# Performance work log

Hardware: AMD Instinct MI355X
Metric: run time of the kernel (lower is better)

The kernel has to match this reference:

```python
import jax, jax.numpy as jnp
import numpy as np

S_LOCAL = 3
N_HEADS = 8
EPS = 1e-6


def setup_inputs() -> dict:
    key = jax.random.key(0)
    ks = jax.random.split(key, 9)
    B, D, T, H, W = 2, 512, 96, 16, 16
    std = 0.02
    return {
        "x": jax.random.normal(ks[0], (B, D, T, H, W), dtype=jnp.float32),
        "ln_gamma": jnp.ones((D,), dtype=jnp.float32),
        "ln_beta": jnp.zeros((D,), dtype=jnp.float32),
        "Wq": jax.random.normal(ks[1], (D, D), dtype=jnp.float32) * std,
        "Wk": jax.random.normal(ks[2], (D, D), dtype=jnp.float32) * std,
        "Wv": jax.random.normal(ks[3], (D, D), dtype=jnp.float32) * std,
        "Wkl": jax.random.normal(ks[4], (D, D), dtype=jnp.float32) * std,
        "Wvl": jax.random.normal(ks[5], (D, D), dtype=jnp.float32) * std,
        "Wo": jax.random.normal(ks[6], (D, D), dtype=jnp.float32) * std,
        "q_bias": jax.random.normal(ks[7], (1, N_HEADS, 1, D // N_HEADS), dtype=jnp.float32) * std,
    }


def _unfold_windows(x, s):
    # x: [..., T] -> [..., T, s] sliding windows with zero padding s//2 each side
    p = s // 2
    xp = jnp.pad(x, [(0, 0)] * (x.ndim - 1) + [(p, p)])
    T = x.shape[-1]
    idx = jnp.arange(T)[:, None] + jnp.arange(s)[None, :]  # [T, s]
    return xp[..., idx]


def reference(x, ln_gamma, ln_beta, Wq, Wk, Wv, Wkl, Wvl, Wo, q_bias):
    B, D, T, H, W = x.shape
    nh, dh, s = N_HEADS, D // N_HEADS, S_LOCAL
    factor = dh ** (-0.5)
    N = B * H * W

    # [B,D,T,H,W] -> [N, T, D]
    xt = jnp.transpose(x, (0, 3, 4, 2, 1)).reshape(N, T, D)

    # LayerNorm over D
    mu = xt.mean(-1, keepdims=True)
    var = xt.var(-1, keepdims=True)
    xn = (xt - mu) / jnp.sqrt(var + EPS) * ln_gamma + ln_beta

    # projections -> [N, nh, T, dh]
    def heads(y):
        return jnp.transpose(y.reshape(N, T, nh, dh), (0, 2, 1, 3))

    q = heads(xn @ Wq.T) + q_bias
    k = heads(xn @ Wk.T)
    v = heads(xn @ Wv.T)

    # global attention scores [N, nh, T, T]
    attn_global = jnp.einsum('bhnd,bhgd->bhng', q, k) * factor

    # local k/v: [N, T, D] -> [N, D, T] -> windows [N, D, T, s]
    kl = jnp.transpose(xn @ Wkl.T, (0, 2, 1))
    vl = jnp.transpose(xn @ Wvl.T, (0, 2, 1))
    k_w = jnp.transpose(_unfold_windows(kl, s).reshape(N, nh, dh, T, s), (0, 1, 3, 2, 4))  # [N,nh,T,dh,s]
    v_w = jnp.transpose(_unfold_windows(vl, s).reshape(N, nh, dh, T, s), (0, 1, 3, 2, 4))

    # local mask: True where window element came from zero padding -> [T, s]
    mask_local = _unfold_windows(jnp.ones((T,), dtype=jnp.float32), s) == 0

    attn_local = jnp.einsum('bhnd,bhndl->bhnl', q, k_w)
    attn_local = jnp.where(mask_local, -jnp.inf, attn_local) * factor

    # joint softmax over [T global + s local]
    attn_map = jax.nn.softmax(jnp.concatenate([attn_global, attn_local], axis=-1), axis=-1)
    ag, al = attn_map[..., :T], attn_map[..., T:]

    x_global = jnp.einsum('bhng,bhgd->bhnd', ag, v)
    x_local = jnp.einsum('bhnl,bhndl->bhnd', al, v_w)

    out = (jnp.transpose(x_global + x_local, (0, 2, 1, 3)).reshape(N, T, D)) @ Wo.T
    return jnp.transpose(out.reshape(B, H, W, T, D), (0, 4, 3, 1, 2))
```

## Files before the change

kernel.cpp:

```cpp
#include <hip/hip_runtime.h>
#include <hip/hip_fp16.h>
#include <cstdint>
#include <cstddef>

typedef _Float16 f16;
typedef _Float16 half8 __attribute__((ext_vector_type(8)));
typedef _Float16 half4v __attribute__((ext_vector_type(4)));
typedef float floatx4 __attribute__((ext_vector_type(4)));

#define MTOT 49152

__device__ __forceinline__ void gload_lds16(const f16* g, f16* l) {
  __builtin_amdgcn_global_load_lds((const __attribute__((address_space(1))) void*)g,
                                   (__attribute__((address_space(3))) void*)l, 16, 0, 0);
}

__device__ __forceinline__ half8 load_h8u(const f16* p) {
  half8 v;
  __builtin_memcpy(&v, p, 16);
  return v;
}

__global__ __launch_bounds__(256) void wconv_kernel(
    const float* __restrict__ Wq, const float* __restrict__ Wk,
    const float* __restrict__ Wv, const float* __restrict__ Wkl,
    const float* __restrict__ Wvl, const float* __restrict__ Wo,
    f16* __restrict__ WQKV, f16* __restrict__ WO) {
  int idx = blockIdx.x * 256 + threadIdx.x;
  if (idx < 2560 * 512) {
    int row = idx >> 9;
    int col = idx & 511;
    int seg = row >> 9;
    int r = row & 511;
    const float* src;
    switch (seg) {
      case 0: src = Wq; break;
      case 1: src = Wk; break;
      case 2: src = Wkl; break;
      case 3: src = Wvl; break;
      default: src = Wv; break;
    }
    WQKV[idx] = (f16)src[r * 512 + col];
  }
  if (idx < 512 * 512) WO[idx] = (f16)Wo[idx];
}

__global__ __launch_bounds__(256) void ln_kernel(
    const float* __restrict__ x, const float* __restrict__ gamma,
    const float* __restrict__ beta, f16* __restrict__ XN) {
  const int hwg = blockIdx.x & 3;
  const int t   = (blockIdx.x >> 2) % 96;
  const int b   = blockIdx.x / (4 * 96);
  const int lhw = threadIdx.x & 63;
  const int dg  = threadIdx.x >> 6;
  const int hw  = hwg * 64 + lhw;
  const float* xp = x + (size_t)b * 512 * 24576 + (size_t)t * 256 + hw;

  float s = 0.f, s2 = 0.f;
  for (int d = dg * 128; d < dg * 128 + 128; ++d) {
    float v = xp[(size_t)d * 24576];
    s += v;
    s2 += v * v;
  }
  __shared__ float S1[4][64], S2[4][64];
  S1[dg][lhw] = s;
  S2[dg][lhw] = s2;
  __syncthreads();
  s  = S1[0][lhw] + S1[1][lhw] + S1[2][lhw] + S1[3][lhw];
  s2 = S2[0][lhw] + S2[1][lhw] + S2[2][lhw] + S2[3][lhw];
  const float mean = s * (1.f / 512.f);
  float var = s2 * (1.f / 512.f) - mean * mean;
  var = fmaxf(var, 0.f);
  const float rstd = rsqrtf(var + 1e-6f);
  const int n = b * 256 + hw;
  f16* outp = XN + ((size_t)n * 96 + t) * 512;
  for (int d0 = dg * 128; d0 < dg * 128 + 128; d0 += 8) {
    half8 buf;
#pragma unroll
    for (int j = 0; j < 8; ++j) {
      float v = xp[(size_t)(d0 + j) * 24576];
      buf[j] = (f16)((v - mean) * rstd * gamma[d0 + j] + beta[d0 + j]);
    }
    *(half8*)(outp + d0) = buf;
  }
}

template <int EPI>
__global__ __launch_bounds__(256) void gemm_kernel(
    const f16* __restrict__ A, const f16* __restrict__ B,
    f16* __restrict__ Cqkv, f16* __restrict__ VT, f16* __restrict__ VLT,
    const float* __restrict__ qbias, float* __restrict__ Out) {
  __shared__ f16 As[2][128 * 32];
  __shared__ f16 Bs[2][128 * 32];
  __shared__ f16 esc[4][16][20];

  const int lin = blockIdx.x;
  const int cpx = (int)gridDim.x >> 3;
  const int o = (lin & 7) * cpx + (lin >> 3);
  int mt, nt;
  if (EPI == 0) {
    mt = o / 20;
    nt = o % 20;
  } else {
    nt = o >> 2;
    mt = o & 3;
  }
  const int m0 = mt * 128;
  const int n0 = nt * 128;
  const int tid = threadIdx.x;
  const int lane = tid & 63;
  const int wid = tid >> 6;
  const int wm = wid >> 1, wn = wid & 1;
  const int l15 = lane & 15, l4 = lane >> 4;

  floatx4 acc[4][4] = {};

  const int srow = tid >> 2;
  const int skp = (((tid & 3) ^ ((tid >> 3) & 3))) * 8;
  const f16* ap = A + (size_t)(m0 + srow) * 512 + skp;
  const f16* bp = B + (size_t)(n0 + srow) * 512 + skp;

  auto stage = [&](int buf, int k0) {
    f16* asl = As[buf] + tid * 8;
    f16* bsl = Bs[buf] + tid * 8;
    gload_lds16(ap + k0, asl);
    gload_lds16(ap + (size_t)64 * 512 + k0, asl + 2048);
    gload_lds16(bp + k0, bsl);
    gload_lds16(bp + (size_t)64 * 512 + k0, bsl + 2048);
  };

  const int rc = (l4 ^ ((l15 >> 1) & 3)) * 8;

  stage(0, 0);
  __syncthreads();
  int cur = 0;
  for (int k0 = 0; k0 < 512; k0 += 32) {
    if (k0 + 32 < 512) stage(cur ^ 1, k0 + 32);
    half8 af[4], bf[4];
#pragma unroll
    for (int mf = 0; mf < 4; ++mf)
      af[mf] = *(const half8*)(As[cur] + (wm * 64 + mf * 16 + l15) * 32 + rc);
#pragma unroll
    for (int nf = 0; nf < 4; ++nf)
      bf[nf] = *(const half8*)(Bs[cur] + (wn * 64 + nf * 16 + l15) * 32 + rc);
#pragma unroll
    for (int mf = 0; mf < 4; ++mf)
#pragma unroll
      for (int nf = 0; nf < 4; ++nf)
        acc[mf][nf] = __builtin_amdgcn_mfma_f32_16x16x32_f16(af[mf], bf[nf], acc[mf][nf], 0, 0, 0);
    __syncthreads();
    cur ^= 1;
  }

  const int mbase = m0 + wm * 64;
  const int nbase = n0 + wn * 64;
  if (EPI == 0) {
#pragma unroll
    for (int nf = 0; nf < 4; ++nf) {
      const int n = nbase + nf * 16 + l15;
      if (nbase + nf * 16 < 1536) {
        const float bias = (n < 512) ? qbias[n] : 0.0f;
#pragma unroll
        for (int mf = 0; mf < 4; ++mf) {
#pragma unroll
          for (int j = 0; j < 4; ++j)
            esc[wid][l4 * 4 + j][l15] = (f16)(acc[mf][nf][j] + bias);
          asm volatile("s_waitcnt lgkmcnt(0)" ::: "memory");
          half4v vv = *(const half4v*)(&esc[wid][l15][l4 * 4]);
          *(half4v*)(Cqkv + (size_t)(mbase + mf * 16 + l15) * 1536 + nbase + nf * 16 + l4 * 4) = vv;
          asm volatile("s_waitcnt lgkmcnt(0)" ::: "memory");
        }
      } else {
        f16* dst = (n < 2048) ? VLT : VT;
        const int i = (n < 2048) ? (n - 1536) : (n - 2048);
#pragma unroll
        for (int mf = 0; mf < 4; ++mf) {
          const int mr = mbase + mf * 16 + l4 * 4;
          const int nn = mr / 96;
          const int t = mr % 96;
          half4v v;
#pragma unroll
          for (int j = 0; j < 4; ++j) v[j] = (f16)acc[mf][nf][j];
          *(half4v*)(dst + ((size_t)nn * 512 + i) * 96 + t) = v;
        }
      }
    }
  } else {
#pragma unroll
    for (int nf = 0; nf < 4; ++nf) {
      const int m2 = nbase + nf * 16 + l15;
      const int bb = m2 / 24576;
      const int rem = m2 - bb * 24576;
      const int t = rem >> 8;
      const int hw = rem & 255;
      float* op = Out + ((size_t)bb * 512 * 96 + t) * 256 + hw;
#pragma unroll
      for (int mf = 0; mf < 4; ++mf) {
#pragma unroll
        for (int j = 0; j < 4; ++j) {
          const int d = mbase + mf * 16 + l4 * 4 + j;
          op[(size_t)d * 24576] = acc[mf][nf][j];
        }
      }
    }
  }
}

__global__ __launch_bounds__(64) void attn_kernel(
    const f16* __restrict__ QKV, const f16* __restrict__ VT,
    const f16* __restrict__ VLT, f16* __restrict__ AO, int n0chunk) {
  const int nn = blockIdx.x >> 3;
  const int h = blockIdx.x & 7;
  const int mb0 = blockIdx.y * 2;
  const int lane = threadIdx.x;
  const int l15 = lane & 15, l4 = lane >> 4;
  const int nglob = n0chunk + nn;
  const int bb = nglob >> 8, hw = nglob & 255;

  __shared__ __align__(16) float locS[16][4];
  __shared__ __align__(16) f16 pS[16][104];
  __shared__ __align__(16) f16 pS2[16][40];

  const f16* base = QKV + (size_t)nn * 96 * 1536;
  const f16* vtb  = VT  + ((size_t)nn * 512 + h * 64) * 96;
  const f16* vltb = VLT + ((size_t)nn * 512 + h * 64) * 96;

  half8 kb[6][2];
#pragma unroll
  for (int nf = 0; nf < 6; ++nf)
#pragma unroll
    for (int kg = 0; kg < 2; ++kg)
      kb[nf][kg] = *(const half8*)(base + (size_t)(nf * 16 + l15) * 1536 + 512 + h * 64 + kg * 32 + l4 * 8);

  for (int mb = mb0; mb < mb0 + 2; ++mb) {
    const int t0 = mb * 16;
    const int tb = (t0 >= 2) ? (t0 - 2) : 0;
    const int d0 = t0 - 1 - tb;

    half8 aq[2], kl1[2], kl2[2];
    {
      int r1 = t0 - 1 + l15; if (r1 < 0) r1 = 0;
      int r2 = t0 + 1 + l15; if (r2 > 95) r2 = 95;
#pragma unroll
      for (int kg = 0; kg < 2; ++kg) {
        aq[kg]  = *(const half8*)(base + (size_t)(t0 + l15) * 1536 + h * 64 + kg * 32 + l4 * 8);
        kl1[kg] = *(const half8*)(base + (size_t)r1 * 1536 + 1024 + h * 64 + kg * 32 + l4 * 8);
        kl2[kg] = *(const half8*)(base + (size_t)r2 * 1536 + 1024 + h * 64 + kg * 32 + l4 * 8);
      }
    }

    floatx4 s[6] = {};
    floatx4 sl1 = {}, sl2 = {};
#pragma unroll
    for (int nf = 0; nf < 6; ++nf)
#pragma unroll
      for (int kg = 0; kg < 2; ++kg)
        s[nf] = __builtin_amdgcn_mfma_f32_16x16x32_f16(aq[kg], kb[nf][kg], s[nf], 0, 0, 0);
#pragma unroll
    for (int kg = 0; kg < 2; ++kg) {
      sl1 = __builtin_amdgcn_mfma_f32_16x16x32_f16(aq[kg], kl1[kg], sl1, 0, 0, 0);
      sl2 = __builtin_amdgcn_mfma_f32_16x16x32_f16(aq[kg], kl2[kg], sl2, 0, 0, 0);
    }

    half8 vb[4][3], vlb[4];
#pragma unroll
    for (int nf = 0; nf < 4; ++nf) {
#pragma unroll
      for (int kg = 0; kg < 3; ++kg)
        vb[nf][kg] = *(const half8*)(vtb + (size_t)(nf * 16 + l15) * 96 + kg * 32 + l4 * 8);
      vlb[nf] = load_h8u(vltb + (size_t)(nf * 16 + l15) * 96 + tb + l4 * 8);
    }

    {
      half8 z = {};
      f16* pz = &pS2[0][0];
      *(half8*)(pz + lane * 8) = z;
      if (lane < 16) *(half8*)(pz + 512 + lane * 8) = z;
    }
#pragma unroll
    for (int j = 0; j < 4; ++j) {
      const int r = l4 * 4 + j;
      const int s1i = l15 - r;
      if (s1i >= 0 && s1i < 3) locS[r][s1i] = sl1[j] * 0.125f;
      const int s2i = l15 + 2 - r;
      if (l15 >= 14 && s2i >= 0 && s2i < 3) locS[r][s2i] = sl2[j] * 0.125f;
    }
    __syncthreads();

#pragma unroll
    for (int j = 0; j < 4; ++j) {
      const int row = l4 * 4 + j;
      float sv[6];
#pragma unroll
      for (int nf = 0; nf < 6; ++nf) sv[nf] = s[nf][j] * 0.125f;
      float mx = sv[0];
#pragma unroll
      for (int nf = 1; nf < 6; ++nf) mx = fmaxf(mx, sv[nf]);
      for (int off = 1; off < 16; off <<= 1) mx = fmaxf(mx, __shfl_xor(mx, off, 64));
      const float l0 = (t0 + row >= 1)  ? locS[row][0] : -__builtin_inff();
      const float l1 = locS[row][1];
      const float l2 = (t0 + row <= 94) ? locS[row][2] : -__builtin_inff();
      mx = fmaxf(mx, fmaxf(l0, fmaxf(l1, l2)));
      float e[6], sum = 0.f;
#pragma unroll
      for (int nf = 0; nf < 6; ++nf) {
        e[nf] = expf(sv[nf] - mx);
        sum += e[nf];
      }
      for (int off = 1; off < 16; off <<= 1) sum += __shfl_xor(sum, off, 64);
      const float e0 = expf(l0 - mx), e1 = expf(l1 - mx), e2 = expf(l2 - mx);
      sum += e0 + e1 + e2;
      const float rd = 1.0f / sum;
#pragma unroll
      for (int nf = 0; nf < 6; ++nf) pS[row][nf * 16 + l15] = (f16)(e[nf] * rd);
      if (l15 < 3) {
        const int w = row + l15 + d0;
        const float ev = (l15 == 0) ? e0 : ((l15 == 1) ? e1 : e2);
        if (w >= 0) pS2[row][w] = (f16)(ev * rd);
      }
    }
    __syncthreads();

    floatx4 o[4] = {};
    half8 pfr[3];
#pragma unroll
    for (int kg = 0; kg < 3; ++kg)
      pfr[kg] = *(const half8*)(&pS[l15][kg * 32 + l4 * 8]);
    half8 pf2 = *(const half8*)(&pS2[l15][l4 * 8]);
#pragma unroll
    for (int nf = 0; nf < 4; ++nf) {
#pragma unroll
      for (int kg = 0; kg < 3; ++kg)
        o[nf] = __builtin_amdgcn_mfma_f32_16x16x32_f16(pfr[kg], vb[nf][kg], o[nf], 0, 0, 0);
      o[nf] = __builtin_amdgcn_mfma_f32_16x16x32_f16(pf2, vlb[nf], o[nf], 0, 0, 0);
    }

#pragma unroll
    for (int nf = 0; nf < 4; ++nf) {
      const int col = h * 64 + nf * 16 + l15;
#pragma unroll
      for (int j = 0; j < 4; ++j) {
        const int t = t0 + l4 * 4 + j;
        AO[((size_t)(bb * 96 + t) * 256 + hw) * 512 + col] = (f16)o[nf][j];
      }
    }
    __syncthreads();
  }
}

extern "C" void kernel_launch(void* const* d_in, const int* in_sizes, int n_in,
                              void* d_out, int out_size, void* d_ws, size_t ws_size,
                              hipStream_t stream) {
  (void)in_sizes; (void)n_in; (void)out_size;
  const float* x     = (const float*)d_in[0];
  const float* gamma = (const float*)d_in[1];
  const float* beta  = (const float*)d_in[2];
  const float* Wq    = (const float*)d_in[3];
  const float* Wk    = (const float*)d_in[4];
  const float* Wv    = (const float*)d_in[5];
  const float* Wkl   = (const float*)d_in[6];
  const float* Wvl   = (const float*)d_in[7];
  const float* Wo    = (const float*)d_in[8];
  const float* qb    = (const float*)d_in[9];
  float* out = (float*)d_out;

  char* ws = (char*)d_ws;
  size_t off = 0;
  auto alloc = [&](size_t bytes) -> void* {
    void* p = ws + off;
    off += (bytes + 255) & ~(size_t)255;
    return p;
  };
  f16* XN   = (f16*)alloc((size_t)MTOT * 512 * 2);
  f16* AO   = (f16*)alloc((size_t)MTOT * 512 * 2);
  f16* WQKV = (f16*)alloc((size_t)2560 * 512 * 2);
  f16* WOh  = (f16*)alloc((size_t)512 * 512 * 2);
  int cn = 512;
  while (cn > 4 &&
         off + (size_t)cn * 96 * 1536 * 2 + 256 + (size_t)cn * 512 * 96 * 2 + 256 +
                 (size_t)cn * 512 * 96 * 2 + 512 > ws_size)
    cn >>= 1;
  f16* QKVc = (f16*)alloc((size_t)cn * 96 * 1536 * 2);
  f16* VTc  = (f16*)alloc((size_t)cn * 512 * 96 * 2);
  f16* VLTc = (f16*)alloc((size_t)cn * 512 * 96 * 2 + 256);

  wconv_kernel<<<5120, 256, 0, stream>>>(Wq, Wk, Wv, Wkl, Wvl, Wo, WQKV, WOh);
  ln_kernel<<<768, 256, 0, stream>>>(x, gamma, beta, XN);
  hipMemsetAsync((char*)VLTc + (size_t)cn * 512 * 96 * 2, 0, 256, stream);

  const int nch = 512 / cn;
  for (int c = 0; c < nch; ++c) {
    const int ng1 = (cn * 96 / 128) * 20;
    gemm_kernel<0><<<ng1, 256, 0, stream>>>(XN + (size_t)c * cn * 96 * 512, WQKV,
                                            QKVc, VTc, VLTc, qb, nullptr);
    attn_kernel<<<dim3(cn * 8, 3), 64, 0, stream>>>(QKVc, VTc, VLTc, AO, c * cn);
  }
  gemm_kernel<1><<<1536, 256, 0, stream>>>(WOh, AO, nullptr, nullptr, nullptr, nullptr, out);
}
```

Measured before the change: 472.9 us.

## Store V/VL row-major in QKV and transpose in LDS inside attention

The projection GEMM now writes all five projections (Q, K, KL, VL, V) row-major into one 2560-wide buffer. It folds the 1/8 softmax scale into Q along with the bias, and uses plain per-element stores in place of the LDS-staged transpose epilogue. The attention kernel moves from 64-thread blocks over a 3-wide grid to 192-thread blocks, one per (n, head). Each block cooperatively loads V and VL for its head, transposes them into shared memory, and the three waves each handle two query tiles. This removes the strided transposed global writes and the separate VT/VLT buffers, at the cost of scalar 2-byte global stores in the GEMM epilogue and LDS transpose work.

```diff
diff --git a/kernel.cpp b/kernel.cpp
--- a/kernel.cpp
+++ b/kernel.cpp
@@ -88,11 +88,10 @@
 template <int EPI>
 __global__ __launch_bounds__(256) void gemm_kernel(
     const f16* __restrict__ A, const f16* __restrict__ B,
-    f16* __restrict__ Cqkv, f16* __restrict__ VT, f16* __restrict__ VLT,
-    const float* __restrict__ qbias, float* __restrict__ Out) {
+    f16* __restrict__ Cqkv, const float* __restrict__ qbias,
+    float* __restrict__ Out) {
   __shared__ f16 As[2][128 * 32];
   __shared__ f16 Bs[2][128 * 32];
-  __shared__ f16 esc[4][16][20];
 
   const int lin = blockIdx.x;
   const int cpx = (int)gridDim.x >> 3;
@@ -158,31 +157,15 @@
 #pragma unroll
     for (int nf = 0; nf < 4; ++nf) {
       const int n = nbase + nf * 16 + l15;
-      if (nbase + nf * 16 < 1536) {
-        const float bias = (n < 512) ? qbias[n] : 0.0f;
-#pragma unroll
-        for (int mf = 0; mf < 4; ++mf) {
-#pragma unroll
-          for (int j = 0; j < 4; ++j)
-            esc[wid][l4 * 4 + j][l15] = (f16)(acc[mf][nf][j] + bias);
-          asm volatile("s_waitcnt lgkmcnt(0)" ::: "memory");
-          half4v vv = *(const half4v*)(&esc[wid][l15][l4 * 4]);
-          *(half4v*)(Cqkv + (size_t)(mbase + mf * 16 + l15) * 1536 + nbase + nf * 16 + l4 * 4) = vv;
-          asm volatile("s_waitcnt lgkmcnt(0)" ::: "memory");
-        }
-      } else {
-        f16* dst = (n < 2048) ? VLT : VT;
-        const int i = (n < 2048) ? (n - 1536) : (n - 2048);
-#pragma unroll
-        for (int mf = 0; mf < 4; ++mf) {
-          const int mr = mbase + mf * 16 + l4 * 4;
-          const int nn = mr / 96;
-          const int t = mr % 96;
-          half4v v;
-#pragma unroll
-          for (int j = 0; j < 4; ++j) v[j] = (f16)acc[mf][nf][j];
-          *(half4v*)(dst + ((size_t)nn * 512 + i) * 96 + t) = v;
-        }
+      const bool isq = (n < 512);
+      const float bias = isq ? qbias[n] : 0.0f;
+      const float scl = isq ? 0.125f : 1.0f;
+#pragma unroll
+      for (int mf = 0; mf < 4; ++mf) {
+        const int mr = mbase + mf * 16 + l4 * 4;
+#pragma unroll
+        for (int j = 0; j < 4; ++j)
+          Cqkv[(size_t)(mr + j) * 2560 + n] = (f16)((acc[mf][nf][j] + bias) * scl);
       }
     }
   } else {
@@ -206,33 +189,52 @@
   }
 }
 
-__global__ __launch_bounds__(64) void attn_kernel(
-    const f16* __restrict__ QKV, const f16* __restrict__ VT,
-    const f16* __restrict__ VLT, f16* __restrict__ AO, int n0chunk) {
+__global__ __launch_bounds__(192) void attn_kernel(
+    const f16* __restrict__ QKV, f16* __restrict__ AO, int n0chunk) {
   const int nn = blockIdx.x >> 3;
   const int h = blockIdx.x & 7;
-  const int mb0 = blockIdx.y * 2;
-  const int lane = threadIdx.x;
+  const int tid = threadIdx.x;
+  const int wid = tid >> 6;
+  const int lane = tid & 63;
   const int l15 = lane & 15, l4 = lane >> 4;
   const int nglob = n0chunk + nn;
   const int bb = nglob >> 8, hw = nglob & 255;
 
-  __shared__ __align__(16) float locS[16][4];
-  __shared__ __align__(16) f16 pS[16][104];
-  __shared__ __align__(16) f16 pS2[16][40];
-
-  const f16* base = QKV + (size_t)nn * 96 * 1536;
-  const f16* vtb  = VT  + ((size_t)nn * 512 + h * 64) * 96;
-  const f16* vltb = VLT + ((size_t)nn * 512 + h * 64) * 96;
+  __shared__ __align__(16) f16 VTl[64][112];
+  __shared__ __align__(16) f16 VLTl[64][112];
+  __shared__ __align__(16) float locS[3][16][4];
+  __shared__ __align__(16) f16 pS[3][16][104];
+  __shared__ __align__(16) f16 pS2[3][16][40];
+
+  const f16* base = QKV + (size_t)nn * 96 * 2560;
+
+#pragma unroll
+  for (int it = 0; it < 4; ++it) {
+    const int r = (tid >> 3) + it * 24;
+    const int c0 = (tid & 7) * 8;
+    half8 v  = *(const half8*)(base + (size_t)r * 2560 + 2048 + h * 64 + c0);
+    half8 vl = *(const half8*)(base + (size_t)r * 2560 + 1536 + h * 64 + c0);
+#pragma unroll
+    for (int j = 0; j < 8; ++j) {
+      VTl[c0 + j][r]  = v[j];
+      VLTl[c0 + j][r] = vl[j];
+    }
+  }
+  if (tid < 128) {
+    half8 z = {};
+    *(half8*)(&VLTl[tid >> 1][96 + (tid & 1) * 8]) = z;
+  }
 
   half8 kb[6][2];
 #pragma unroll
   for (int nf = 0; nf < 6; ++nf)
 #pragma unroll
     for (int kg = 0; kg < 2; ++kg)
-      kb[nf][kg] = *(const half8*)(base + (size_t)(nf * 16 + l15) * 1536 + 512 + h * 64 + kg * 32 + l4 * 8);
-
-  for (int mb = mb0; mb < mb0 + 2; ++mb) {
+      kb[nf][kg] = *(const half8*)(base + (size_t)(nf * 16 + l15) * 2560 + 512 + h * 64 + kg * 32 + l4 * 8);
+
+  __syncthreads();
+
+  for (int mb = wid * 2; mb < wid * 2 + 2; ++mb) {
     const int t0 = mb * 16;
     const int tb = (t0 >= 2) ? (t0 - 2) : 0;
     const int d0 = t0 - 1 - tb;
@@ -243,9 +245,9 @@
       int r2 = t0 + 1 + l15; if (r2 > 95) r2 = 95;
 #pragma unroll
       for (int kg = 0; kg < 2; ++kg) {
-        aq[kg]  = *(const half8*)(base + (size_t)(t0 + l15) * 1536 + h * 64 + kg * 32 + l4 * 8);
-        kl1[kg] = *(const half8*)(base + (size_t)r1 * 1536 + 1024 + h * 64 + kg * 32 + l4 * 8);
-        kl2[kg] = *(const half8*)(base + (size_t)r2 * 1536 + 1024 + h * 64 + kg * 32 + l4 * 8);
+        aq[kg]  = *(const half8*)(base + (size_t)(t0 + l15) * 2560 + h * 64 + kg * 32 + l4 * 8);
+        kl1[kg] = *(const half8*)(base + (size_t)r1 * 2560 + 1024 + h * 64 + kg * 32 + l4 * 8);
+        kl2[kg] = *(const half8*)(base + (size_t)r2 * 2560 + 1024 + h * 64 + kg * 32 + l4 * 8);
       }
     }
 
@@ -267,13 +269,13 @@
     for (int nf = 0; nf < 4; ++nf) {
 #pragma unroll
       for (int kg = 0; kg < 3; ++kg)
-        vb[nf][kg] = *(const half8*)(vtb + (size_t)(nf * 16 + l15) * 96 + kg * 32 + l4 * 8);
-      vlb[nf] = load_h8u(vltb + (size_t)(nf * 16 + l15) * 96 + tb + l4 * 8);
+        vb[nf][kg] = *(const half8*)(&VTl[nf * 16 + l15][kg * 32 + l4 * 8]);
+      vlb[nf] = load_h8u(&VLTl[nf * 16 + l15][tb + l4 * 8]);
     }
 
     {
       half8 z = {};
-      f16* pz = &pS2[0][0];
+      f16* pz = &pS2[wid][0][0];
       *(half8*)(pz + lane * 8) = z;
       if (lane < 16) *(half8*)(pz + 512 + lane * 8) = z;
     }
@@ -281,9 +283,9 @@
     for (int j = 0; j < 4; ++j) {
       const int r = l4 * 4 + j;
       const int s1i = l15 - r;
-      if (s1i >= 0 && s1i < 3) locS[r][s1i] = sl1[j] * 0.125f;
+      if (s1i >= 0 && s1i < 3) locS[wid][r][s1i] = sl1[j];
       const int s2i = l15 + 2 - r;
-      if (l15 >= 14 && s2i >= 0 && s2i < 3) locS[r][s2i] = sl2[j] * 0.125f;
+      if (l15 >= 14 && s2i >= 0 && s2i < 3) locS[wid][r][s2i] = sl2[j];
     }
     __syncthreads();
 
@@ -292,14 +294,14 @@
       const int row = l4 * 4 + j;
       float sv[6];
 #pragma unroll
-      for (int nf = 0; nf < 6; ++nf) sv[nf] = s[nf][j] * 0.125f;
+      for (int nf = 0; nf < 6; ++nf) sv[nf] = s[nf][j];
       float mx = sv[0];
 #pragma unroll
       for (int nf = 1; nf < 6; ++nf) mx = fmaxf(mx, sv[nf]);
       for (int off = 1; off < 16; off <<= 1) mx = fmaxf(mx, __shfl_xor(mx, off, 64));
-      const float l0 = (t0 + row >= 1)  ? locS[row][0] : -__builtin_inff();
-      const float l1 = locS[row][1];
-      const float l2 = (t0 + row <= 94) ? locS[row][2] : -__builtin_inff();
+      const float l0 = (t0 + row >= 1)  ? locS[wid][row][0] : -__builtin_inff();
+      const float l1 = locS[wid][row][1];
+      const float l2 = (t0 + row <= 94) ? locS[wid][row][2] : -__builtin_inff();
       mx = fmaxf(mx, fmaxf(l0, fmaxf(l1, l2)));
       float e[6], sum = 0.f;
 #pragma unroll
@@ -312,11 +314,11 @@
       sum += e0 + e1 + e2;
       const float rd = 1.0f / sum;
 #pragma unroll
-      for (int nf = 0; nf < 6; ++nf) pS[row][nf * 16 + l15] = (f16)(e[nf] * rd);
+      for (int nf = 0; nf < 6; ++nf) pS[wid][row][nf * 16 + l15] = (f16)(e[nf] * rd);
       if (l15 < 3) {
         const int w = row + l15 + d0;
         const float ev = (l15 == 0) ? e0 : ((l15 == 1) ? e1 : e2);
-        if (w >= 0) pS2[row][w] = (f16)(ev * rd);
+        if (w >= 0) pS2[wid][row][w] = (f16)(ev * rd);
       }
     }
     __syncthreads();
@@ -325,8 +327,8 @@
     half8 pfr[3];
 #pragma unroll
     for (int kg = 0; kg < 3; ++kg)
-      pfr[kg] = *(const half8*)(&pS[l15][kg * 32 + l4 * 8]);
-    half8 pf2 = *(const half8*)(&pS2[l15][l4 * 8]);
+      pfr[kg] = *(const half8*)(&pS[wid][l15][kg * 32 + l4 * 8]);
+    half8 pf2 = *(const half8*)(&pS2[wid][l15][l4 * 8]);
 #pragma unroll
     for (int nf = 0; nf < 4; ++nf) {
 #pragma unroll
@@ -344,7 +346,6 @@
         AO[((size_t)(bb * 96 + t) * 256 + hw) * 512 + col] = (f16)o[nf][j];
       }
     }
-    __syncthreads();
   }
 }
 
@@ -376,24 +377,19 @@
   f16* WQKV = (f16*)alloc((size_t)2560 * 512 * 2);
   f16* WOh  = (f16*)alloc((size_t)512 * 512 * 2);
   int cn = 512;
-  while (cn > 4 &&
-         off + (size_t)cn * 96 * 1536 * 2 + 256 + (size_t)cn * 512 * 96 * 2 + 256 +
-                 (size_t)cn * 512 * 96 * 2 + 512 > ws_size)
+  while (cn > 4 && off + (size_t)cn * 96 * 2560 * 2 + 256 > ws_size)
     cn >>= 1;
-  f16* QKVc = (f16*)alloc((size_t)cn * 96 * 1536 * 2);
-  f16* VTc  = (f16*)alloc((size_t)cn * 512 * 96 * 2);
-  f16* VLTc = (f16*)alloc((size_t)cn * 512 * 96 * 2 + 256);
+  f16* QKVc = (f16*)alloc((size_t)cn * 96 * 2560 * 2);
 
   wconv_kernel<<<5120, 256, 0, stream>>>(Wq, Wk, Wv, Wkl, Wvl, Wo, WQKV, WOh);
   ln_kernel<<<768, 256, 0, stream>>>(x, gamma, beta, XN);
-  hipMemsetAsync((char*)VLTc + (size_t)cn * 512 * 96 * 2, 0, 256, stream);
 
   const int nch = 512 / cn;
   for (int c = 0; c < nch; ++c) {
     const int ng1 = (cn * 96 / 128) * 20;
     gemm_kernel<0><<<ng1, 256, 0, stream>>>(XN + (size_t)c * cn * 96 * 512, WQKV,
-                                            QKVc, VTc, VLTc, qb, nullptr);
-    attn_kernel<<<dim3(cn * 8, 3), 64, 0, stream>>>(QKVc, VTc, VLTc, AO, c * cn);
-  }
-  gemm_kernel<1><<<1536, 256, 0, stream>>>(WOh, AO, nullptr, nullptr, nullptr, nullptr, out);
-}
+                                            QKVc, qb, nullptr);
+    attn_kernel<<<cn * 8, 192, 0, stream>>>(QKVc, AO, c * cn);
+  }
+  gemm_kernel<1><<<1536, 256, 0, stream>>>(WOh, AO, nullptr, nullptr, out);
+}
```

Result: faster. 443.1 us (-6.3%).
